# Performance work log

Measured on AMD Instinct MI355X. Metric: run time of the kernel, lower is better.

## Reference

```python
import jax, jax.numpy as jnp
import numpy as np

B, IN, H = 4096, 1024, 1024


def setup_inputs() -> dict:
    key = jax.random.key(0)
    ks = jax.random.split(key, 6)
    s_h = 1.0 / np.sqrt(H)
    s_x = 1.0 / np.sqrt(IN)
    return {
        "x": jax.random.normal(ks[0], (B, IN), jnp.float32),
        "h": jax.random.normal(ks[1], (B, H), jnp.float32),
        "c": jax.random.normal(ks[2], (B, H), jnp.float32),
        # hidden_lin: Linear(H, 4H) with bias
        "Wh": jax.random.uniform(ks[3], (4 * H, H), jnp.float32, -s_h, s_h),
        "bh": jax.random.uniform(ks[4], (4 * H,), jnp.float32, -s_h, s_h),
        # input_lin: Linear(IN, 4H), bias=False
        "Wx": jax.random.uniform(ks[5], (4 * H, IN), jnp.float32, -s_x, s_x),
    }


def reference(x, h, c, Wh, bh, Wx):
    # ifgo = h @ Wh^T + bh + x @ Wx^T   -> [B, 4H]
    ifgo = jnp.dot(h, Wh.T) + bh + jnp.dot(x, Wx.T)
    i, f, g, o = jnp.split(ifgo, 4, axis=1)
    i = jax.nn.sigmoid(i)
    f = jax.nn.sigmoid(f)
    g = jnp.tanh(g)
    o = jax.nn.sigmoid(o)
    c_next = f * c + i * g
    h_next = o * jnp.tanh(c_next)
    return (h_next, c_next)
```

## Files before the change

kernel.cpp:

```cpp
#include <hip/hip_runtime.h>
#include <cstdint>
#include <cstddef>


#define NB   4096
#define KH   1024
#define NOUT 4096
#define ARR_ELEMS 4194304

typedef __bf16 bf16x8 __attribute__((ext_vector_type(8)));
typedef float  f32x4  __attribute__((ext_vector_type(4)));

__device__ inline unsigned short f2bf(float f) {
    union { float f; unsigned int u; } v; v.f = f;
    unsigned int u = v.u;
    u += 0x7FFFu + ((u >> 16) & 1u);
    return (unsigned short)(u >> 16);
}

__device__ inline float fsig(float v)  { return __builtin_amdgcn_rcpf(1.f + __expf(-v)); }
__device__ inline float ftanh(float v) { return 1.f - 2.f * __builtin_amdgcn_rcpf(1.f + __expf(2.f * v)); }

__global__ void convert_kernel(const float* __restrict__ h, const float* __restrict__ x,
                               const float* __restrict__ Wh, const float* __restrict__ Wx,
                               unsigned short* __restrict__ dst) {
    int idx = blockIdx.x * 256 + threadIdx.x;
    int arr = idx >> 20;
    int off = (idx & 0xFFFFF) << 2;
    const float* src = (arr == 0) ? h : (arr == 1) ? x : (arr == 2) ? Wh : Wx;
    float4 v = *(const float4*)(src + off);
    unsigned int lo = (unsigned int)f2bf(v.x) | ((unsigned int)f2bf(v.y) << 16);
    unsigned int hi = (unsigned int)f2bf(v.z) | ((unsigned int)f2bf(v.w) << 16);
    uint2 packed; packed.x = lo; packed.y = hi;

    int dstOff = off;
    if (arr >= 2) {
        int L   = off >> 10;
        int col = off & 1023;
        int g = L >> 10, j = L & 1023;
        int p = ((j >> 4) << 6) | (g << 4) | (j & 15);
        dstOff = (p << 10) | col;
    }
    *(uint2*)(dst + (size_t)arr * ARR_ELEMS + dstOff) = packed;
}

__global__ void gemm_kernel(const unsigned short* __restrict__ Ah,
                            const unsigned short* __restrict__ Ax,
                            const unsigned short* __restrict__ Bh,
                            const unsigned short* __restrict__ Bx,
                            const float* __restrict__ bh,
                            const float* __restrict__ c,
                            float* __restrict__ out) {
    __shared__ __align__(16) unsigned short As[128 * 32];
    __shared__ __align__(16) unsigned short Bs[128 * 32];

    const int tid  = threadIdx.x;
    const int wave = tid >> 6;
    const int lane = tid & 63;
    const int tileN = blockIdx.x;
    const int tileM = blockIdx.y;

    const int stRow  = wave * 16 + (lane >> 2);
    const int stColE = (lane & 3) * 8;
    const size_t gaRow = (size_t)(tileM * 128 + stRow) * KH;
    const size_t gbRow = (size_t)(tileN * 128 + stRow) * KH;

    const int mBase = (wave >> 1) * 64;
    const int nBase = (wave & 1) * 64;
    const int fr = lane & 15;
    const int fk = (lane >> 4) * 8;

    f32x4 acc[4][4] = {};

    for (int kt = 0; kt < 64; ++kt) {
        const unsigned short* Aseg = (kt < 32) ? Ah : Ax;
        const unsigned short* Bseg = (kt < 32) ? Bh : Bx;
        const int kk = (kt & 31) * 32;

        const unsigned short* ga0 = Aseg + gaRow + kk + stColE;
        const unsigned short* gb0 = Bseg + gbRow + kk + stColE;
        __builtin_amdgcn_global_load_lds(
            (const __attribute__((address_space(1))) void*)ga0,
            (__attribute__((address_space(3))) void*)(As + wave * 512), 16, 0, 0);
        __builtin_amdgcn_global_load_lds(
            (const __attribute__((address_space(1))) void*)(ga0 + 64 * KH),
            (__attribute__((address_space(3))) void*)(As + 2048 + wave * 512), 16, 0, 0);
        __builtin_amdgcn_global_load_lds(
            (const __attribute__((address_space(1))) void*)gb0,
            (__attribute__((address_space(3))) void*)(Bs + wave * 512), 16, 0, 0);
        __builtin_amdgcn_global_load_lds(
            (const __attribute__((address_space(1))) void*)(gb0 + 64 * KH),
            (__attribute__((address_space(3))) void*)(Bs + 2048 + wave * 512), 16, 0, 0);

        __syncthreads();

        bf16x8 a[4], b[4];
        #pragma unroll
        for (int i = 0; i < 4; ++i)
            a[i] = *(const bf16x8*)(As + (mBase + i * 16 + fr) * 32 + fk);
        #pragma unroll
        for (int j = 0; j < 4; ++j)
            b[j] = *(const bf16x8*)(Bs + (nBase + j * 16 + fr) * 32 + fk);

        #pragma unroll
        for (int i = 0; i < 4; ++i)
            #pragma unroll
            for (int j = 0; j < 4; ++j)
                acc[i][j] = __builtin_amdgcn_mfma_f32_16x16x32_bf16(a[i], b[j], acc[i][j], 0, 0, 0);

        __syncthreads();
    }

    const int j = ((tileN * 2 + (wave & 1)) << 4) | (lane & 15);
    const float bi = bh[j];
    const float bf = bh[j + 1024];
    const float bg = bh[j + 2048];
    const float bo = bh[j + 3072];

    const int row0 = tileM * 128 + mBase + (lane >> 4) * 4;

    float cv[4][4];
    #pragma unroll
    for (int i = 0; i < 4; ++i)
        #pragma unroll
        for (int r = 0; r < 4; ++r)
            cv[i][r] = c[(size_t)(row0 + i * 16 + r) * KH + j];

    #pragma unroll
    for (int i = 0; i < 4; ++i) {
        #pragma unroll
        for (int r = 0; r < 4; ++r) {
            const size_t idx = (size_t)(row0 + i * 16 + r) * KH + j;
            float iv = fsig(acc[i][0][r] + bi);
            float fv = fsig(acc[i][1][r] + bf);
            float gv = ftanh(acc[i][2][r] + bg);
            float ov = fsig(acc[i][3][r] + bo);
            float cn = fv * cv[i][r] + iv * gv;
            float hn = ov * ftanh(cn);
            out[idx] = hn;
            out[(size_t)ARR_ELEMS + idx] = cn;
        }
    }
}

extern "C" void kernel_launch(void* const* d_in, const int* in_sizes, int n_in,
                              void* d_out, int out_size, void* d_ws, size_t ws_size,
                              hipStream_t stream) {
    const float* x  = (const float*)d_in[0];
    const float* h  = (const float*)d_in[1];
    const float* c  = (const float*)d_in[2];
    const float* Wh = (const float*)d_in[3];
    const float* bh = (const float*)d_in[4];
    const float* Wx = (const float*)d_in[5];
    float* out = (float*)d_out;

    unsigned short* ws  = (unsigned short*)d_ws;
    unsigned short* Ahb = ws;
    unsigned short* Axb = ws + 1 * (size_t)ARR_ELEMS;
    unsigned short* Whb = ws + 2 * (size_t)ARR_ELEMS;
    unsigned short* Wxb = ws + 3 * (size_t)ARR_ELEMS;

    convert_kernel<<<16384, 256, 0, stream>>>(h, x, Wh, Wx, ws);
    dim3 grid(NOUT / 128, NB / 128);
    gemm_kernel<<<grid, 256, 0, stream>>>(Ahb, Axb, Whb, Wxb, bh, c, out);
}
```

Before: 206.0 us.

## Concatenate activations and weights along K and remap blocks per XCD

The convert kernel now writes h|x and Wh|Wx into single row-concatenated bf16 buffers of width 2048, so the GEMM streams one contiguous K=2048 row with simple pointer increments and no per-iteration segment selection. Block indices are also remapped so each XCD (blk&7) owns a band of 4 M-tiles and sweeps N. This is meant to improve L2 reuse of A rows within each XCD's cache. The risk is that the remap lowers reuse of B tiles across XCDs, and the strided writes in the convert step could change its write efficiency.

```diff
diff --git a/kernel.cpp b/kernel.cpp
--- a/kernel.cpp
+++ b/kernel.cpp
@@ -5,7 +5,7 @@
 
 #define NB   4096
 #define KH   1024
-#define NOUT 4096
+#define KK   2048
 #define ARR_ELEMS 4194304
 
 typedef __bf16 bf16x8 __attribute__((ext_vector_type(8)));
@@ -23,7 +23,7 @@
 
 __global__ void convert_kernel(const float* __restrict__ h, const float* __restrict__ x,
                                const float* __restrict__ Wh, const float* __restrict__ Wx,
-                               unsigned short* __restrict__ dst) {
+                               unsigned short* __restrict__ A, unsigned short* __restrict__ W) {
     int idx = blockIdx.x * 256 + threadIdx.x;
     int arr = idx >> 20;
     int off = (idx & 0xFFFFF) << 2;
@@ -33,21 +33,24 @@
     unsigned int hi = (unsigned int)f2bf(v.z) | ((unsigned int)f2bf(v.w) << 16);
     uint2 packed; packed.x = lo; packed.y = hi;
 
-    int dstOff = off;
-    if (arr >= 2) {
-        int L   = off >> 10;
-        int col = off & 1023;
-        int g = L >> 10, j = L & 1023;
+    int row = off >> 10;
+    int col = off & 1023;
+    unsigned short* dst;
+    size_t dstOff;
+    if (arr < 2) {
+        dst = A;
+        dstOff = (size_t)row * KK + (arr == 1 ? 1024 : 0) + col;
+    } else {
+        int g = row >> 10, j = row & 1023;
         int p = ((j >> 4) << 6) | (g << 4) | (j & 15);
-        dstOff = (p << 10) | col;
+        dst = W;
+        dstOff = (size_t)p * KK + (arr == 3 ? 1024 : 0) + col;
     }
-    *(uint2*)(dst + (size_t)arr * ARR_ELEMS + dstOff) = packed;
+    *(uint2*)(dst + dstOff) = packed;
 }
 
-__global__ void gemm_kernel(const unsigned short* __restrict__ Ah,
-                            const unsigned short* __restrict__ Ax,
-                            const unsigned short* __restrict__ Bh,
-                            const unsigned short* __restrict__ Bx,
+__global__ void gemm_kernel(const unsigned short* __restrict__ A,
+                            const unsigned short* __restrict__ W,
                             const float* __restrict__ bh,
                             const float* __restrict__ c,
                             float* __restrict__ out) {
@@ -57,13 +60,17 @@
     const int tid  = threadIdx.x;
     const int wave = tid >> 6;
     const int lane = tid & 63;
-    const int tileN = blockIdx.x;
-    const int tileM = blockIdx.y;
+
+    const int blk   = blockIdx.y * 32 + blockIdx.x;
+    const int xcd   = blk & 7;
+    const int sidx  = blk >> 3;
+    const int tileM = xcd * 4 + (sidx & 3);
+    const int tileN = sidx >> 2;
 
     const int stRow  = wave * 16 + (lane >> 2);
     const int stColE = (lane & 3) * 8;
-    const size_t gaRow = (size_t)(tileM * 128 + stRow) * KH;
-    const size_t gbRow = (size_t)(tileN * 128 + stRow) * KH;
+    const unsigned short* ga = A + (size_t)(tileM * 128 + stRow) * KK + stColE;
+    const unsigned short* gb = W + (size_t)(tileN * 128 + stRow) * KK + stColE;
 
     const int mBase = (wave >> 1) * 64;
     const int nBase = (wave & 1) * 64;
@@ -72,24 +79,18 @@
 
     f32x4 acc[4][4] = {};
 
-    for (int kt = 0; kt < 64; ++kt) {
-        const unsigned short* Aseg = (kt < 32) ? Ah : Ax;
-        const unsigned short* Bseg = (kt < 32) ? Bh : Bx;
-        const int kk = (kt & 31) * 32;
-
-        const unsigned short* ga0 = Aseg + gaRow + kk + stColE;
-        const unsigned short* gb0 = Bseg + gbRow + kk + stColE;
+    for (int kt = 0; kt < 64; ++kt, ga += 32, gb += 32) {
         __builtin_amdgcn_global_load_lds(
-            (const __attribute__((address_space(1))) void*)ga0,
+            (const __attribute__((address_space(1))) void*)ga,
             (__attribute__((address_space(3))) void*)(As + wave * 512), 16, 0, 0);
         __builtin_amdgcn_global_load_lds(
-            (const __attribute__((address_space(1))) void*)(ga0 + 64 * KH),
+            (const __attribute__((address_space(1))) void*)(ga + 64 * KK),
             (__attribute__((address_space(3))) void*)(As + 2048 + wave * 512), 16, 0, 0);
         __builtin_amdgcn_global_load_lds(
-            (const __attribute__((address_space(1))) void*)gb0,
+            (const __attribute__((address_space(1))) void*)gb,
             (__attribute__((address_space(3))) void*)(Bs + wave * 512), 16, 0, 0);
         __builtin_amdgcn_global_load_lds(
-            (const __attribute__((address_space(1))) void*)(gb0 + 64 * KH),
+            (const __attribute__((address_space(1))) void*)(gb + 64 * KK),
             (__attribute__((address_space(3))) void*)(Bs + 2048 + wave * 512), 16, 0, 0);
 
         __syncthreads();
@@ -154,13 +155,11 @@
     const float* Wx = (const float*)d_in[5];
     float* out = (float*)d_out;
 
-    unsigned short* ws  = (unsigned short*)d_ws;
-    unsigned short* Ahb = ws;
-    unsigned short* Axb = ws + 1 * (size_t)ARR_ELEMS;
-    unsigned short* Whb = ws + 2 * (size_t)ARR_ELEMS;
-    unsigned short* Wxb = ws + 3 * (size_t)ARR_ELEMS;
+    unsigned short* ws   = (unsigned short*)d_ws;
+    unsigned short* Acat = ws;
+    unsigned short* Wcat = ws + 2 * (size_t)ARR_ELEMS;
 
-    convert_kernel<<<16384, 256, 0, stream>>>(h, x, Wh, Wx, ws);
-    dim3 grid(NOUT / 128, NB / 128);
-    gemm_kernel<<<grid, 256, 0, stream>>>(Ahb, Axb, Whb, Wxb, bh, c, out);
+    convert_kernel<<<16384, 256, 0, stream>>>(h, x, Wh, Wx, Acat, Wcat);
+    dim3 grid(32, 32);
+    gemm_kernel<<<grid, 256, 0, stream>>>(Acat, Wcat, bh, c, out);
 }
```

Result: no change. 208.7 us (+1.3%).
